# Kernel tuning notes

Hardware: AMD Instinct MI355X
Metric: run time of the kernel (lower is better)

Reference implementation:

```python
import jax, jax.numpy as jnp
import numpy as np

SIG_DEPTH = 4  # matches sig_depth init arg


def _outer(a, b):
    # flattened tensor product: [B, m] x [B, n] -> [B, m*n] (row-major, matches signatory layout)
    return (a[:, :, None] * b[:, None, :]).reshape(a.shape[0], -1)


def setup_inputs() -> dict:
    key = jax.random.key(0)
    k1, k2 = jax.random.split(key)
    B, L, Cin = 64, 256, 7
    out_dim = 512
    C = Cin + 1
    sig_channels = sum(C ** k for k in range(1, SIG_DEPTH + 1))  # 4680
    inp = jax.random.normal(k1, (B, L, Cin), dtype=jnp.float32)
    W = jax.random.normal(k2, (out_dim, sig_channels), dtype=jnp.float32) * 0.02
    b = jnp.zeros((out_dim,), dtype=jnp.float32)
    return {"inp": inp, "W": W, "b": b}


def reference(inp, W, b):
    B, L, Cin = inp.shape
    # Augment: prepend time channel linspace(0, 1, L), keep original channels
    t = jnp.broadcast_to(jnp.linspace(0.0, 1.0, L, dtype=inp.dtype)[None, :, None], (B, L, 1))
    x = jnp.concatenate([t, inp], axis=-1)  # [B, L, C]
    C = Cin + 1
    d = SIG_DEPTH
    dx = jnp.transpose(x[:, 1:] - x[:, :-1], (1, 0, 2))  # [L-1, B, C] increments
    init = tuple(jnp.zeros((B, C ** (k + 1)), x.dtype) for k in range(d))  # identity signature (all zero levels)

    def step(levels, v):
        # exp(v) in the truncated tensor algebra: e_k = v^{(x)k} / k!
        e = [v]
        for k in range(1, d):
            e.append(_outer(e[-1], v) / (k + 1))
        # Chen's identity: new_k = a_k + e_k + sum_{i=1}^{k-1} a_i (x) e_{k-i}
        new = []
        for k in range(d):
            acc = levels[k] + e[k]
            for i in range(k):
                acc = acc + _outer(levels[i], e[k - 1 - i])
            new.append(acc)
        sig = jnp.concatenate(new, axis=-1)  # [B, sig_channels]
        return tuple(new), sig

    _, sigs = jax.lax.scan(step, init, dx)  # [L-1, B, sig_channels] (stream=True)
    sigs = jnp.transpose(sigs, (1, 0, 2))   # [B, L-1, sig_channels]
    return sigs @ W.T + b                   # [B, L-1, out_dim]
```

## Files before the change

kernel.cpp:

```cpp
#include <hip/hip_runtime.h>
#include <hip/hip_bf16.h>

#define BATCH 64
#define LSEQ 256
#define CIN 7
#define CC 8
#define NSIG 4680
#define KPAD 4736
#define TSTEPS 255
#define ODIM 512
#define NCHUNK 16
#define CH 16

typedef __attribute__((ext_vector_type(8))) unsigned short ushort8;
typedef __attribute__((ext_vector_type(8))) __bf16 bf16x8;
typedef __attribute__((ext_vector_type(4))) float f32x4;

__device__ __forceinline__ unsigned short f2bf(float x) {
    __hip_bfloat16 h = __float2bfloat16(x);
    return *(unsigned short*)&h;
}

#define GLDS16(gp, lp)                                                      \
    __builtin_amdgcn_global_load_lds(                                       \
        (const __attribute__((address_space(1))) void*)(gp),                \
        (__attribute__((address_space(3))) void*)(lp), 16, 0, 0)

__global__ __launch_bounds__(512) void sig_ckpt_kernel(const float* __restrict__ inp,
                                                       float* __restrict__ ckpt) {
    __shared__ float sDx[TSTEPS * CC];

    const int b   = blockIdx.x;
    const int tid = threadIdx.x;

    const float* ip = inp + (size_t)b * LSEQ * CIN;
    for (int i = tid; i < TSTEPS * CC; i += 512) {
        int t = i >> 3, c = i & 7;
        sDx[i] = (c == 0) ? (1.0f / 255.0f)
                          : ip[(t + 1) * CIN + (c - 1)] - ip[t * CIN + (c - 1)];
    }
    __syncthreads();

    const int i1 = tid >> 6;
    const int i2 = (tid >> 3) & 7;
    const int i3 = tid & 7;

    float a1own = 0.0f, a2own = 0.0f, a3 = 0.0f;
    float a4[8];
#pragma unroll
    for (int e = 0; e < 8; ++e) a4[e] = 0.0f;

    for (int t = 0; t < 240; ++t) {
        const float* v = &sDx[t * CC];
        const float4 vlo = *(const float4*)&v[0];
        const float4 vhi = *(const float4*)&v[4];
        const float va = v[i1], vb = v[i2], vc = v[i3];
        const float e3s = va * vb * vc * (1.0f / 6.0f);
        const float T4 = e3s * 0.25f + a1own * vb * vc * (1.0f / 6.0f)
                       + a2own * vc * 0.5f + a3;
        a4[0] += vlo.x * T4; a4[1] += vlo.y * T4;
        a4[2] += vlo.z * T4; a4[3] += vlo.w * T4;
        a4[4] += vhi.x * T4; a4[5] += vhi.y * T4;
        a4[6] += vhi.z * T4; a4[7] += vhi.w * T4;
        a3 += e3s + (a1own * vb * 0.5f + a2own) * vc;
        a2own += vb * (0.5f * va + a1own);
        a1own += va;

        if (((t + 1) & 15) == 0) {
            const int c = ((t + 1) >> 4) - 1;
            float* cp = ckpt + ((size_t)b * 15 + c) * NSIG;
            if ((tid & 63) == 0) cp[i1] = a1own;
            if ((tid & 7) == 0) cp[8 + (tid >> 3)] = a2own;
            cp[72 + tid] = a3;
            float4 q0 = {a4[0], a4[1], a4[2], a4[3]};
            float4 q1 = {a4[4], a4[5], a4[6], a4[7]};
            *(float4*)&cp[584 + tid * 8]     = q0;
            *(float4*)&cp[584 + tid * 8 + 4] = q1;
        }
    }
}

__global__ __launch_bounds__(512) void sig_write_kernel(const float* __restrict__ inp,
                                                        const float* __restrict__ ckpt,
                                                        unsigned short* __restrict__ sig) {
    __shared__ float sDx[CH * CC];

    const int chunk = blockIdx.x;
    const int b     = blockIdx.y;
    const int tid   = threadIdx.x;
    const int t0    = chunk * CH;
    const int t1    = (chunk == NCHUNK - 1) ? TSTEPS : t0 + CH;

    const float* ip = inp + (size_t)b * LSEQ * CIN;
    for (int i = tid; i < (t1 - t0) * CC; i += 512) {
        int t = t0 + (i >> 3), c = i & 7;
        sDx[i] = (c == 0) ? (1.0f / 255.0f)
                          : ip[(t + 1) * CIN + (c - 1)] - ip[t * CIN + (c - 1)];
    }
    __syncthreads();

    const int i1 = tid >> 6;
    const int i2 = (tid >> 3) & 7;
    const int i3 = tid & 7;

    float a1own, a2own, a3;
    float a4[8];
    if (chunk == 0) {
        a1own = a2own = a3 = 0.0f;
#pragma unroll
        for (int e = 0; e < 8; ++e) a4[e] = 0.0f;
    } else {
        const float* cp = ckpt + ((size_t)b * 15 + (chunk - 1)) * NSIG;
        a1own = cp[i1];
        a2own = cp[8 + (tid >> 3)];
        a3    = cp[72 + tid];
        float4 q0 = *(const float4*)&cp[584 + tid * 8];
        float4 q1 = *(const float4*)&cp[584 + tid * 8 + 4];
        a4[0] = q0.x; a4[1] = q0.y; a4[2] = q0.z; a4[3] = q0.w;
        a4[4] = q1.x; a4[5] = q1.y; a4[6] = q1.z; a4[7] = q1.w;
    }

    for (int t = t0; t < t1; ++t) {
        const float* v = &sDx[(t - t0) * CC];
        const float4 vlo = *(const float4*)&v[0];
        const float4 vhi = *(const float4*)&v[4];
        const float va = v[i1], vb = v[i2], vc = v[i3];
        const float e3s = va * vb * vc * (1.0f / 6.0f);
        const float T4 = e3s * 0.25f + a1own * vb * vc * (1.0f / 6.0f)
                       + a2own * vc * 0.5f + a3;
        a4[0] += vlo.x * T4; a4[1] += vlo.y * T4;
        a4[2] += vlo.z * T4; a4[3] += vlo.w * T4;
        a4[4] += vhi.x * T4; a4[5] += vhi.y * T4;
        a4[6] += vhi.z * T4; a4[7] += vhi.w * T4;
        a3 += e3s + (a1own * vb * 0.5f + a2own) * vc;
        a2own += vb * (0.5f * va + a1own);
        a1own += va;

        unsigned short* row = sig + ((size_t)b * TSTEPS + t) * KPAD;
        ushort8 pack;
#pragma unroll
        for (int e = 0; e < 8; ++e) pack[e] = f2bf(a4[e]);
        *(ushort8*)(row + 584 + tid * 8) = pack;
        row[72 + tid] = f2bf(a3);
        if ((tid & 63) == 0) row[i1] = f2bf(a1own);
        if ((tid & 7) == 0) row[8 + (tid >> 3)] = f2bf(a2own);
        if (tid >= 448 && tid < 504) row[4232 + tid] = 0;
    }
}

__global__ __launch_bounds__(256) void wcvt_kernel(const float* __restrict__ W,
                                                   unsigned short* __restrict__ Wb) {
    int idx = blockIdx.x * 256 + threadIdx.x;
    if (idx >= ODIM * KPAD) return;
    int n = idx / KPAD, k = idx - n * KPAD;
    Wb[idx] = (k < NSIG) ? f2bf(W[(size_t)n * NSIG + k]) : (unsigned short)0;
}

__global__ __launch_bounds__(256) void gemm_kernel(const unsigned short* __restrict__ A,
                                                   const unsigned short* __restrict__ Wb,
                                                   const float* __restrict__ bias,
                                                   float* __restrict__ out,
                                                   int Mrows) {
    __shared__ unsigned short As[128 * 64];
    __shared__ unsigned short Bs[128 * 64];

    const int tid = threadIdx.x;
    int nt, mt;
    if (gridDim.y == 128) {
        const int li = blockIdx.y * 4 + blockIdx.x;
        const int x  = li & 7;
        const int j  = li >> 3;
        mt = x * 16 + (j >> 2);
        nt = j & 3;
    } else {
        nt = blockIdx.x; mt = blockIdx.y;
    }
    const int lane = tid & 63;
    const int wv   = tid >> 6;
    const int wr   = wv >> 1;
    const int wc   = wv & 1;
    const int lr   = lane & 15;
    const int lk   = (lane >> 4) * 8;
    const int sb   = lr & 7;

    const f32x4 z4 = {0.0f, 0.0f, 0.0f, 0.0f};
    f32x4 acc[4][4];
#pragma unroll
    for (int i = 0; i < 4; ++i)
#pragma unroll
        for (int j = 0; j < 4; ++j) acc[i][j] = z4;

    const int srow = tid >> 3;
    const int gcb  = (tid & 7) ^ (srow & 7);
    const int scol = gcb * 8;

    for (int k0 = 0; k0 < KPAD; k0 += 64) {
#pragma unroll
        for (int i = 0; i < 4; ++i) {
            int gr = mt * 128 + i * 32 + srow;
            if (gr >= Mrows) gr = 0;
            GLDS16(A + (size_t)gr * KPAD + k0 + scol,
                   ((char*)As) + i * 4096 + tid * 16);
            const int gn = nt * 128 + i * 32 + srow;
            GLDS16(Wb + (size_t)gn * KPAD + k0 + scol,
                   ((char*)Bs) + i * 4096 + tid * 16);
        }
        __syncthreads();

#pragma unroll
        for (int ks = 0; ks < 2; ++ks) {
            const int kb  = (ks * 32 + lk) >> 3;
            const int kel = (kb ^ sb) * 8;
            bf16x8 af[4], bf[4];
#pragma unroll
            for (int i = 0; i < 4; ++i)
                af[i] = *(const bf16x8*)&As[(wr * 64 + i * 16 + lr) * 64 + kel];
#pragma unroll
            for (int j = 0; j < 4; ++j)
                bf[j] = *(const bf16x8*)&Bs[(wc * 64 + j * 16 + lr) * 64 + kel];
#pragma unroll
            for (int i = 0; i < 4; ++i)
#pragma unroll
                for (int j = 0; j < 4; ++j)
                    acc[i][j] = __builtin_amdgcn_mfma_f32_16x16x32_bf16(
                        af[i], bf[j], acc[i][j], 0, 0, 0);
        }
        __syncthreads();
    }

    float bn[4];
#pragma unroll
    for (int j = 0; j < 4; ++j)
        bn[j] = bias[nt * 128 + wc * 64 + j * 16 + lr];

#pragma unroll
    for (int i = 0; i < 4; ++i) {
        const int mbase = mt * 128 + wr * 64 + i * 16 + (lane >> 4) * 4;
#pragma unroll
        for (int r = 0; r < 4; ++r) {
            const int m = mbase + r;
            if (m < Mrows) {
#pragma unroll
                for (int j = 0; j < 4; ++j) {
                    const int n = nt * 128 + wc * 64 + j * 16 + lr;
                    out[(size_t)m * ODIM + n] = acc[i][j][r] + bn[j];
                }
            }
        }
    }
}

extern "C" void kernel_launch(void* const* d_in, const int* in_sizes, int n_in,
                              void* d_out, int out_size, void* d_ws, size_t ws_size,
                              hipStream_t stream) {
    const float* inp  = (const float*)d_in[0];
    const float* W    = (const float*)d_in[1];
    const float* bias = (const float*)d_in[2];
    float* out = (float*)d_out;

    const size_t wbBytes = (size_t)ODIM * KPAD * sizeof(unsigned short);
    const size_t sigPB   = (size_t)TSTEPS * KPAD * sizeof(unsigned short);
    const size_t ckptPB  = (size_t)15 * NSIG * sizeof(float);
    const size_t perB    = sigPB + ckptPB;

    int nbMax = (int)((ws_size - wbBytes) / perB);
    if (nbMax > BATCH) nbMax = BATCH;
    if (nbMax < 1) nbMax = 1;

    unsigned short* sig  = (unsigned short*)d_ws;
    float*          ckpt = (float*)((char*)d_ws + (size_t)nbMax * sigPB);
    unsigned short* Wb   = (unsigned short*)((char*)d_ws + (ws_size - wbBytes));

    wcvt_kernel<<<(ODIM * KPAD + 255) / 256, 256, 0, stream>>>(W, Wb);

    for (int b0 = 0; b0 < BATCH; b0 += nbMax) {
        const int nb = (b0 + nbMax <= BATCH) ? nbMax : (BATCH - b0);
        const int Mrows = nb * TSTEPS;
        const float* ipb = inp + (size_t)b0 * LSEQ * CIN;
        sig_ckpt_kernel<<<nb, 512, 0, stream>>>(ipb, ckpt);
        sig_write_kernel<<<dim3(NCHUNK, nb), 512, 0, stream>>>(ipb, ckpt, sig);
        gemm_kernel<<<dim3(ODIM / 128, (Mrows + 127) / 128), 256, 0, stream>>>(
            sig, Wb, bias, out + (size_t)b0 * TSTEPS * ODIM, Mrows);
    }
}
```

Before: 166.1 us.

## Enlarge GEMM tile to 256x128 with 512 threads and triple-buffered async LDS loads

Rewrites the GEMM main loop to use a 256x128 block tile with 8 waves and a three-stage LDS ring buffer. Global-to-LDS loads for tile t+2 are issued before computing tile t, with partial vmcnt waits and one barrier per iteration instead of two. The aim is to hide global load latency and raise reuse of the W tile. The cost is much more LDS per block (about 144KB), so only one block fits per CU, and the grid shrinks to 256 blocks.

Result: slower. 176.8 us (+6.5%).

```diff
diff --git a/kernel.cpp b/kernel.cpp
--- a/kernel.cpp
+++ b/kernel.cpp
@@ -11,6 +11,9 @@
 #define ODIM 512
 #define NCHUNK 16
 #define CH 16
+#define NKT 74
+#define BM 256
+#define BN 128
 
 typedef __attribute__((ext_vector_type(8))) unsigned short ushort8;
 typedef __attribute__((ext_vector_type(8))) __bf16 bf16x8;
@@ -156,21 +159,21 @@
     Wb[idx] = (k < NSIG) ? f2bf(W[(size_t)n * NSIG + k]) : (unsigned short)0;
 }
 
-__global__ __launch_bounds__(256) void gemm_kernel(const unsigned short* __restrict__ A,
+__global__ __launch_bounds__(512) void gemm_kernel(const unsigned short* __restrict__ A,
                                                    const unsigned short* __restrict__ Wb,
                                                    const float* __restrict__ bias,
                                                    float* __restrict__ out,
                                                    int Mrows) {
-    __shared__ unsigned short As[128 * 64];
-    __shared__ unsigned short Bs[128 * 64];
+    __shared__ unsigned short As[3][BM * 64];
+    __shared__ unsigned short Bs[3][BN * 64];
 
     const int tid = threadIdx.x;
     int nt, mt;
-    if (gridDim.y == 128) {
+    if (gridDim.y == 64) {
         const int li = blockIdx.y * 4 + blockIdx.x;
         const int x  = li & 7;
         const int j  = li >> 3;
-        mt = x * 16 + (j >> 2);
+        mt = x * 8 + (j >> 2);
         nt = j & 3;
     } else {
         nt = blockIdx.x; mt = blockIdx.y;
@@ -194,19 +197,43 @@
     const int gcb  = (tid & 7) ^ (srow & 7);
     const int scol = gcb * 8;
 
-    for (int k0 = 0; k0 < KPAD; k0 += 64) {
-#pragma unroll
-        for (int i = 0; i < 4; ++i) {
-            int gr = mt * 128 + i * 32 + srow;
-            if (gr >= Mrows) gr = 0;
-            GLDS16(A + (size_t)gr * KPAD + k0 + scol,
-                   ((char*)As) + i * 4096 + tid * 16);
-            const int gn = nt * 128 + i * 32 + srow;
-            GLDS16(Wb + (size_t)gn * KPAD + k0 + scol,
-                   ((char*)Bs) + i * 4096 + tid * 16);
-        }
-        __syncthreads();
-
+    const unsigned short* aptr[4];
+    const unsigned short* bptr[2];
+#pragma unroll
+    for (int i = 0; i < 4; ++i) {
+        int gr = mt * BM + i * 64 + srow;
+        if (gr >= Mrows) gr = 0;
+        aptr[i] = A + (size_t)gr * KPAD + scol;
+    }
+#pragma unroll
+    for (int i = 0; i < 2; ++i)
+        bptr[i] = Wb + (size_t)(nt * BN + i * 64 + srow) * KPAD + scol;
+
+#define STAGE(buf, koff)                                                    \
+    do {                                                                    \
+        _Pragma("unroll")                                                   \
+        for (int i_ = 0; i_ < 4; ++i_)                                      \
+            GLDS16(aptr[i_] + (koff),                                       \
+                   ((char*)As[buf]) + i_ * 8192 + tid * 16);                \
+        _Pragma("unroll")                                                   \
+        for (int i_ = 0; i_ < 2; ++i_)                                      \
+            GLDS16(bptr[i_] + (koff),                                       \
+                   ((char*)Bs[buf]) + i_ * 8192 + tid * 16);                \
+    } while (0)
+
+    STAGE(0, 0);
+    STAGE(1, 64);
+    asm volatile("s_waitcnt vmcnt(6)" ::: "memory");
+    __builtin_amdgcn_sched_barrier(0);
+    __builtin_amdgcn_s_barrier();
+    __builtin_amdgcn_sched_barrier(0);
+
+    int cur = 0, nxt = 1, nn = 2;
+    for (int t = 0; t < NKT; ++t) {
+        if (t + 2 < NKT) STAGE(nn, (t + 2) * 64);
+
+        const unsigned short* as = &As[0][0] + cur * (BM * 64);
+        const unsigned short* bs = &Bs[0][0] + cur * (BN * 64);
 #pragma unroll
         for (int ks = 0; ks < 2; ++ks) {
             const int kb  = (ks * 32 + lk) >> 3;
@@ -214,10 +241,10 @@
             bf16x8 af[4], bf[4];
 #pragma unroll
             for (int i = 0; i < 4; ++i)
-                af[i] = *(const bf16x8*)&As[(wr * 64 + i * 16 + lr) * 64 + kel];
+                af[i] = *(const bf16x8*)&as[(wr * 64 + i * 16 + lr) * 64 + kel];
 #pragma unroll
             for (int j = 0; j < 4; ++j)
-                bf[j] = *(const bf16x8*)&Bs[(wc * 64 + j * 16 + lr) * 64 + kel];
+                bf[j] = *(const bf16x8*)&bs[(wc * 64 + j * 16 + lr) * 64 + kel];
 #pragma unroll
             for (int i = 0; i < 4; ++i)
 #pragma unroll
@@ -225,29 +252,42 @@
                     acc[i][j] = __builtin_amdgcn_mfma_f32_16x16x32_bf16(
                         af[i], bf[j], acc[i][j], 0, 0, 0);
         }
-        __syncthreads();
+
+        if (t + 2 < NKT) {
+            asm volatile("s_waitcnt vmcnt(6)" ::: "memory");
+            __builtin_amdgcn_sched_barrier(0);
+            __builtin_amdgcn_s_barrier();
+            __builtin_amdgcn_sched_barrier(0);
+        } else if (t + 1 < NKT) {
+            asm volatile("s_waitcnt vmcnt(0)" ::: "memory");
+            __builtin_amdgcn_sched_barrier(0);
+            __builtin_amdgcn_s_barrier();
+            __builtin_amdgcn_sched_barrier(0);
+        }
+        const int tmp = cur; cur = nxt; nxt = nn; nn = tmp;
     }
 
     float bn[4];
 #pragma unroll
     for (int j = 0; j < 4; ++j)
-        bn[j] = bias[nt * 128 + wc * 64 + j * 16 + lr];
+        bn[j] = bias[nt * BN + wc * 64 + j * 16 + lr];
 
 #pragma unroll
     for (int i = 0; i < 4; ++i) {
-        const int mbase = mt * 128 + wr * 64 + i * 16 + (lane >> 4) * 4;
+        const int mbase = mt * BM + wr * 64 + i * 16 + (lane >> 4) * 4;
 #pragma unroll
         for (int r = 0; r < 4; ++r) {
             const int m = mbase + r;
             if (m < Mrows) {
 #pragma unroll
                 for (int j = 0; j < 4; ++j) {
-                    const int n = nt * 128 + wc * 64 + j * 16 + lr;
+                    const int n = nt * BN + wc * 64 + j * 16 + lr;
                     out[(size_t)m * ODIM + n] = acc[i][j][r] + bn[j];
                 }
             }
         }
     }
+#undef STAGE
 }
 
 extern "C" void kernel_launch(void* const* d_in, const int* in_sizes, int n_in,
@@ -279,7 +319,7 @@
         const float* ipb = inp + (size_t)b0 * LSEQ * CIN;
         sig_ckpt_kernel<<<nb, 512, 0, stream>>>(ipb, ckpt);
         sig_write_kernel<<<dim3(NCHUNK, nb), 512, 0, stream>>>(ipb, ckpt, sig);
-        gemm_kernel<<<dim3(ODIM / 128, (Mrows + 127) / 128), 256, 0, stream>>>(
+        gemm_kernel<<<dim3(ODIM / BN, (Mrows + BM - 1) / BM), 512, 0, stream>>>(
             sig, Wb, bias, out + (size_t)b0 * TSTEPS * ODIM, Mrows);
     }
 }
```
